# Kernel tuning notes

Measured on AMD Instinct MI355X. Metric: run time of the kernel, lower is better.

## Reference

```python
import jax, jax.numpy as jnp
import numpy as np
import math

N, MA, NFS, K, RC = 4, 256, 128, 8, 5.0
HID, OUT = 256, 32


def setup_inputs() -> dict:
    key = jax.random.key(0)
    ks = jax.random.split(key, 9)
    z = jax.random.randint(ks[0], (N, MA), 0, 10)
    r = jax.random.normal(ks[1], (N, MA, 3), dtype=jnp.float32) * 3.0
    h = jax.random.normal(ks[2], (N, MA, NFS), dtype=jnp.float32)
    Wa = jax.random.normal(ks[3], (2 * NFS, 1), dtype=jnp.float32) * 0.05
    ba = jnp.zeros((1,), dtype=jnp.float32)
    Wp1 = jax.random.normal(ks[4], (2 * NFS, HID), dtype=jnp.float32) * 0.05
    bp1 = jnp.zeros((HID,), dtype=jnp.float32)
    Wp2 = jax.random.normal(ks[5], (HID, OUT), dtype=jnp.float32) * 0.05
    bp2 = jnp.zeros((OUT,), dtype=jnp.float32)
    return {"z": z, "r": r, "h": h, "Wa": Wa, "ba": ba,
            "Wp1": Wp1, "bp1": bp1, "Wp2": Wp2, "bp2": bp2}


def reference(z, r, h, Wa, ba, Wp1, bp1, Wp2, bp2):
    n, ma = z.shape
    nfs = h.shape[2]
    # distance vectors dv[b,i,j] = r[b,j] - r[b,i]  -> [n, ma, ma, 3]
    dv = r[:, None, :, :] - r[:, :, None, :]
    d = jnp.linalg.norm(dv, axis=3)                       # [n, ma, ma]
    eye = jnp.eye(ma, dtype=jnp.float32)
    # cosine cutoff, zeroed on the diagonal
    cf = 0.5 * (jnp.cos(math.pi * jnp.minimum(d, RC) / RC) + 1.0)
    cf = (cf - eye[None])[..., None]                      # [n, ma, ma, 1]
    # pair validity mask (z > -1 marks real atoms), diagonal removed
    m = (z > -1).astype(jnp.float32)                      # [n, ma]
    mask = m[:, None, :] * m[:, :, None] - eye[None]
    mask = jnp.clip(mask, 0.0)[..., None]                 # [n, ma, ma, 1]
    cf = cf * mask
    # pairwise feature tensor u = [h_i, h_j * cf]         # [n, ma, ma, 2*nfs]
    u1 = jnp.broadcast_to(h[:, :, None, :], (n, ma, ma, nfs))
    u2 = h[:, None, :, :] * cf
    u = jnp.concatenate([u1, u2], axis=3)
    # exp attention, masked, normalized over neighbor axis (dim 2)
    g = (u @ Wa + ba) * mask                              # [n, ma, ma, 1]
    g = jnp.exp(g) - (1.0 - mask)
    attention = g / jnp.clip(g.sum(axis=2, keepdims=True), 1e-8)
    # top-k neighbors per query atom
    att, index = jax.lax.top_k(attention[..., 0], K)      # [n, ma, K]
    att = att[..., None]
    # gather neighbor features and distance vectors
    h2 = jnp.take_along_axis(h[:, None, :, :], index[..., None], axis=2)  # [n, ma, K, nfs]
    h1 = jnp.broadcast_to(h[:, :, None, :], (n, ma, K, nfs))
    uk = jnp.concatenate([h1, h2], axis=3) * att          # [n, ma, K, 2*nfs]
    dvk = jnp.take_along_axis(dv, index[..., None], axis=2)               # [n, ma, K, 3]
    dvk = dvk / jnp.clip(jnp.linalg.norm(dvk, axis=3, keepdims=True), 1e-4)
    dvk = dvk[:, :, :, None, :]                           # [n, ma, K, 1, 3]
    # pool MLP then cross with unit direction vectors
    c = jax.nn.silu(uk @ Wp1 + bp1) @ Wp2 + bp2           # [n, ma, K, OUT]
    c = c[..., None] * dvk                                # [n, ma, K, OUT, 3]
    return (z, r, c)
```

## Files before the change

kernel.cpp:

```cpp
#include <hip/hip_runtime.h>
#include <hip/hip_bf16.h>
#include <math.h>

#define NB 4
#define MA 256
#define NFS 128
#define KSEL 8
#define HID 256
#define NOUT 32
#define RCUT 5.0f
#define PI_F 3.14159265358979323846f

__global__ __launch_bounds__(256) void prep_kernel(
    const int* __restrict__ z, const float* __restrict__ r,
    const float* __restrict__ h, const float* __restrict__ Wa,
    const float* __restrict__ Wp1,
    float* __restrict__ out,
    float* __restrict__ a1, float* __restrict__ a2,
    float* __restrict__ P, float* __restrict__ Q) {
  const int b = blockIdx.x;
  const int half = b & 1;
  const int rg = b >> 1;
  const int r0 = 4 * rg;
  const int t = threadIdx.x;
  const int wave = t >> 6, lane = t & 63;
  const int c = t & 63, fq = t >> 6;

  __shared__ __align__(16) float hsh[4][NFS];
  __shared__ __align__(16) float psum[4][4][HID];

  ((float2*)hsh)[t] = ((const float2*)(h + (size_t)r0 * NFS))[t];
  __syncthreads();

  if (half == 0) {
    const float h0 = hsh[wave][lane], h1 = hsh[wave][lane + 64];
    float p1 = h0 * Wa[lane]       + h1 * Wa[lane + 64];
    float p2 = h0 * Wa[NFS + lane] + h1 * Wa[NFS + lane + 64];
#pragma unroll
    for (int off = 32; off > 0; off >>= 1) {
      p1 += __shfl_down(p1, off);
      p2 += __shfl_down(p2, off);
    }
    if (lane == 0) { a1[r0 + wave] = p1; a2[r0 + wave] = p2; }
    if (t < 4)  out[r0 + t] = (float)z[r0 + t];
    if (t < 12) out[NB * MA + r0 * 3 + t] = r[r0 * 3 + t];
  }

  const float* __restrict__ Wbase = Wp1 + (size_t)(half ? NFS : 0) * HID;
  float4 acc[4] = {make_float4(0,0,0,0), make_float4(0,0,0,0),
                   make_float4(0,0,0,0), make_float4(0,0,0,0)};
#pragma unroll 4
  for (int ff = 0; ff < 32; ++ff) {
    const int f = fq * 32 + ff;
    const float4 w = *(const float4*)&Wbase[(size_t)f * HID + 4 * c];
#pragma unroll
    for (int rr = 0; rr < 4; ++rr) {
      const float hv = hsh[rr][f];
      acc[rr].x = fmaf(hv, w.x, acc[rr].x);
      acc[rr].y = fmaf(hv, w.y, acc[rr].y);
      acc[rr].z = fmaf(hv, w.z, acc[rr].z);
      acc[rr].w = fmaf(hv, w.w, acc[rr].w);
    }
  }
#pragma unroll
  for (int rr = 0; rr < 4; ++rr) *(float4*)&psum[fq][rr][4 * c] = acc[rr];
  __syncthreads();

  {
    const int r2 = t >> 6, c2 = t & 63;
    float4 s = *(const float4*)&psum[0][r2][4 * c2];
#pragma unroll
    for (int q = 1; q < 4; ++q) {
      const float4 p = *(const float4*)&psum[q][r2][4 * c2];
      s.x += p.x; s.y += p.y; s.z += p.z; s.w += p.w;
    }
    float* dst = (half ? Q : P) + (size_t)(r0 + r2) * HID + 4 * c2;
    *(float4*)dst = s;
  }
}

__global__ __launch_bounds__(256) void main_kernel(
    const int* __restrict__ z, const float* __restrict__ r,
    const float* __restrict__ a1g, const float* __restrict__ a2g,
    const float* __restrict__ ba,
    const float* __restrict__ Pg, const float* __restrict__ Qg,
    const float* __restrict__ bp1,
    const float* __restrict__ Wp2g, const float* __restrict__ bp2,
    float* __restrict__ out) {
  const int row = blockIdx.x;
  const int n = row >> 8;
  const int i = row & 255;
  const int tid = threadIdx.x;
  const int lane = tid & 63;

  __shared__ float gsh[MA];
  __shared__ __align__(16) float hid_sh[KSEL][HID];
  __shared__ float psum2[8][KSEL][NOUT];

  const int l2o = tid & 31;
  const int l2c = tid >> 5;
  float wreg[32];
#pragma unroll
  for (int j = 0; j < 32; ++j) wreg[j] = Wp2g[(size_t)(32 * l2c + j) * NOUT + l2o];

  const float rix = r[row * 3 + 0], riy = r[row * 3 + 1], riz = r[row * 3 + 2];
  {
    const int jg = n * MA + tid;
    const float dx = r[jg * 3 + 0] - rix;
    const float dy = r[jg * 3 + 1] - riy;
    const float dz = r[jg * 3 + 2] - riz;
    const float d = sqrtf(dx * dx + dy * dy + dz * dz);
    const int mi = (z[row] > -1) ? 1 : 0;
    const int mj = (z[jg] > -1) ? 1 : 0;
    const int mask = max(mi * mj - ((tid == i) ? 1 : 0), 0);
    float g = 0.0f;
    if (mask) {
      const float cf = 0.5f * (__cosf(PI_F * fminf(d, RCUT) / RCUT) + 1.0f);
      g = __expf(a1g[row] + cf * a2g[jg] + ba[0]);
    }
    gsh[tid] = g;
  }
  __syncthreads();

  float att[KSEL];
  int   idx[KSEL];
  {
    float v0 = gsh[lane];
    float v1 = gsh[lane + 64];
    float v2 = gsh[lane + 128];
    float v3 = gsh[lane + 192];
    float s = (v0 + v1) + (v2 + v3);
#pragma unroll
    for (int off = 32; off > 0; off >>= 1) s += __shfl_xor(s, off);
    const float rden = 1.0f / fmaxf(s, 1e-8f);
#pragma unroll
    for (int k = 0; k < KSEL; k++) {
      float bv = v0; int bi = lane;
      if (v1 > bv) { bv = v1; bi = lane + 64; }
      if (v2 > bv) { bv = v2; bi = lane + 128; }
      if (v3 > bv) { bv = v3; bi = lane + 192; }
#pragma unroll
      for (int off = 32; off > 0; off >>= 1) {
        const float ov = __shfl_xor(bv, off);
        const int oi = __shfl_xor(bi, off);
        if (ov > bv || (ov == bv && oi < bi)) { bv = ov; bi = oi; }
      }
      att[k] = bv * rden;
      idx[k] = __builtin_amdgcn_readfirstlane(bi);
      const int slot = bi >> 6, who = bi & 63;
      if (lane == who) {
        if (slot == 0) v0 = -1.0f;
        else if (slot == 1) v1 = -1.0f;
        else if (slot == 2) v2 = -1.0f;
        else v3 = -1.0f;
      }
    }
  }

  {
    const float pi = Pg[(size_t)row * HID + tid];
    const float bb = bp1[tid];
#pragma unroll
    for (int k = 0; k < KSEL; k++) {
      const float q = Qg[(size_t)(n * MA + idx[k]) * HID + tid];
      const float x = att[k] * (pi + q) + bb;
      hid_sh[k][tid] = x / (1.0f + __expf(-x));
    }
  }
  __syncthreads();

  {
    float acc[KSEL];
#pragma unroll
    for (int k = 0; k < KSEL; ++k) acc[k] = 0.0f;
#pragma unroll
    for (int k = 0; k < KSEL; ++k) {
      const float4* __restrict__ hrow = (const float4*)&hid_sh[k][32 * l2c];
#pragma unroll
      for (int j4 = 0; j4 < 8; ++j4) {
        const float4 hv = hrow[j4];
        acc[k] = fmaf(hv.x, wreg[4 * j4 + 0],
                 fmaf(hv.y, wreg[4 * j4 + 1],
                 fmaf(hv.z, wreg[4 * j4 + 2],
                 fmaf(hv.w, wreg[4 * j4 + 3], acc[k]))));
      }
    }
#pragma unroll
    for (int k = 0; k < KSEL; ++k) psum2[l2c][k][l2o] = acc[k];
  }
  __syncthreads();

  {
    const int k2 = tid >> 5;
    const int o = tid & 31;
    float s = bp2[o];
#pragma unroll
    for (int cc = 0; cc < 8; ++cc) s += psum2[cc][k2][o];
    const int jg = n * MA + idx[k2];
    const float dx = r[jg * 3 + 0] - rix;
    const float dy = r[jg * 3 + 1] - riy;
    const float dz = r[jg * 3 + 2] - riz;
    const float nrm = fmaxf(sqrtf(dx * dx + dy * dy + dz * dz), 1e-4f);
    float* cb = out + NB * MA + NB * MA * 3 +
                ((size_t)row * KSEL + k2) * (NOUT * 3) + o * 3;
    cb[0] = s * (dx / nrm);
    cb[1] = s * (dy / nrm);
    cb[2] = s * (dz / nrm);
  }
}

extern "C" void kernel_launch(void* const* d_in, const int* in_sizes, int n_in,
                              void* d_out, int out_size, void* d_ws, size_t ws_size,
                              hipStream_t stream) {
  const int*   z   = (const int*)d_in[0];
  const float* r   = (const float*)d_in[1];
  const float* h   = (const float*)d_in[2];
  const float* Wa  = (const float*)d_in[3];
  const float* ba  = (const float*)d_in[4];
  const float* Wp1 = (const float*)d_in[5];
  const float* bp1 = (const float*)d_in[6];
  const float* Wp2 = (const float*)d_in[7];
  const float* bp2 = (const float*)d_in[8];
  float* out = (float*)d_out;

  float* a1 = (float*)d_ws;
  float* a2 = a1 + NB * MA;
  float* P  = a2 + NB * MA;
  float* Q  = P + (size_t)NB * MA * HID;

  prep_kernel<<<2 * NB * MA / 4, 256, 0, stream>>>(z, r, h, Wa, Wp1, out, a1, a2, P, Q);
  main_kernel<<<NB * MA, 256, 0, stream>>>(z, r, a1, a2, ba, P, Q, bp1, Wp2, bp2, out);
}
```

Baseline: 22.91 us.

## Double block counts in prep and main kernels by splitting columns and top-k halves

The prep kernel now splits each row group's output columns into two halves, giving four blocks per row group instead of two. The main kernel now launches two blocks per query row, and each block computes the MLP and output for four of the eight selected neighbors. The aim is more parallelism on a GPU with many CUs. In exchange, the attention scores, the softmax sum and the top-k selection are computed redundantly in both halves, and the second half still walks all eight selection rounds.

```diff
diff --git a/kernel.cpp b/kernel.cpp
--- a/kernel.cpp
+++ b/kernel.cpp
@@ -19,20 +19,21 @@
     float* __restrict__ a1, float* __restrict__ a2,
     float* __restrict__ P, float* __restrict__ Q) {
   const int b = blockIdx.x;
-  const int half = b & 1;
-  const int rg = b >> 1;
+  const int colhalf = b & 1;
+  const int pq = (b >> 1) & 1;
+  const int rg = b >> 2;
   const int r0 = 4 * rg;
   const int t = threadIdx.x;
   const int wave = t >> 6, lane = t & 63;
-  const int c = t & 63, fq = t >> 6;
+  const int c = t & 31, fq = t >> 5;
 
   __shared__ __align__(16) float hsh[4][NFS];
-  __shared__ __align__(16) float psum[4][4][HID];
+  __shared__ __align__(16) float psum[8][4][128];
 
   ((float2*)hsh)[t] = ((const float2*)(h + (size_t)r0 * NFS))[t];
   __syncthreads();
 
-  if (half == 0) {
+  if (pq == 0 && colhalf == 0) {
     const float h0 = hsh[wave][lane], h1 = hsh[wave][lane + 64];
     float p1 = h0 * Wa[lane]       + h1 * Wa[lane + 64];
     float p2 = h0 * Wa[NFS + lane] + h1 * Wa[NFS + lane + 64];
@@ -46,12 +47,12 @@
     if (t < 12) out[NB * MA + r0 * 3 + t] = r[r0 * 3 + t];
   }
 
-  const float* __restrict__ Wbase = Wp1 + (size_t)(half ? NFS : 0) * HID;
+  const float* __restrict__ Wbase = Wp1 + (size_t)(pq ? NFS : 0) * HID + colhalf * 128;
   float4 acc[4] = {make_float4(0,0,0,0), make_float4(0,0,0,0),
                    make_float4(0,0,0,0), make_float4(0,0,0,0)};
 #pragma unroll 4
-  for (int ff = 0; ff < 32; ++ff) {
-    const int f = fq * 32 + ff;
+  for (int ff = 0; ff < 16; ++ff) {
+    const int f = fq * 16 + ff;
     const float4 w = *(const float4*)&Wbase[(size_t)f * HID + 4 * c];
 #pragma unroll
     for (int rr = 0; rr < 4; ++rr) {
@@ -68,14 +69,14 @@
 
   {
     const int r2 = t >> 6, c2 = t & 63;
-    float4 s = *(const float4*)&psum[0][r2][4 * c2];
-#pragma unroll
-    for (int q = 1; q < 4; ++q) {
-      const float4 p = *(const float4*)&psum[q][r2][4 * c2];
-      s.x += p.x; s.y += p.y; s.z += p.z; s.w += p.w;
-    }
-    float* dst = (half ? Q : P) + (size_t)(r0 + r2) * HID + 4 * c2;
-    *(float4*)dst = s;
+    float2 s = *(const float2*)&psum[0][r2][2 * c2];
+#pragma unroll
+    for (int q = 1; q < 8; ++q) {
+      const float2 p = *(const float2*)&psum[q][r2][2 * c2];
+      s.x += p.x; s.y += p.y;
+    }
+    float* dst = (pq ? Q : P) + (size_t)(r0 + r2) * HID + colhalf * 128 + 2 * c2;
+    *(float2*)dst = s;
   }
 }
 
@@ -87,15 +88,17 @@
     const float* __restrict__ bp1,
     const float* __restrict__ Wp2g, const float* __restrict__ bp2,
     float* __restrict__ out) {
-  const int row = blockIdx.x;
+  const int row = blockIdx.x >> 1;
+  const int khalf = blockIdx.x & 1;
   const int n = row >> 8;
   const int i = row & 255;
   const int tid = threadIdx.x;
   const int lane = tid & 63;
 
   __shared__ float gsh[MA];
-  __shared__ __align__(16) float hid_sh[KSEL][HID];
-  __shared__ float psum2[8][KSEL][NOUT];
+  __shared__ __align__(16) float hid_sh[4][HID];
+  __shared__ float psum2[8][4][NOUT];
+  __shared__ int   idx_sh[4];
 
   const int l2o = tid & 31;
   const int l2c = tid >> 5;
@@ -122,8 +125,8 @@
   }
   __syncthreads();
 
-  float att[KSEL];
-  int   idx[KSEL];
+  float att4[4];
+  int   idx4[4];
   {
     float v0 = gsh[lane];
     float v1 = gsh[lane + 64];
@@ -135,46 +138,54 @@
     const float rden = 1.0f / fmaxf(s, 1e-8f);
 #pragma unroll
     for (int k = 0; k < KSEL; k++) {
-      float bv = v0; int bi = lane;
-      if (v1 > bv) { bv = v1; bi = lane + 64; }
-      if (v2 > bv) { bv = v2; bi = lane + 128; }
-      if (v3 > bv) { bv = v3; bi = lane + 192; }
-#pragma unroll
-      for (int off = 32; off > 0; off >>= 1) {
-        const float ov = __shfl_xor(bv, off);
-        const int oi = __shfl_xor(bi, off);
-        if (ov > bv || (ov == bv && oi < bi)) { bv = ov; bi = oi; }
+      if (k < 4 || khalf == 1) {
+        float bv = v0; int bi = lane;
+        if (v1 > bv) { bv = v1; bi = lane + 64; }
+        if (v2 > bv) { bv = v2; bi = lane + 128; }
+        if (v3 > bv) { bv = v3; bi = lane + 192; }
+#pragma unroll
+        for (int off = 32; off > 0; off >>= 1) {
+          const float ov = __shfl_xor(bv, off);
+          const int oi = __shfl_xor(bi, off);
+          if (ov > bv || (ov == bv && oi < bi)) { bv = ov; bi = oi; }
+        }
+        if ((k >> 2) == khalf) {
+          att4[k & 3] = bv * rden;
+          idx4[k & 3] = __builtin_amdgcn_readfirstlane(bi);
+        }
+        const int slot = bi >> 6, who = bi & 63;
+        if (lane == who) {
+          if (slot == 0) v0 = -1.0f;
+          else if (slot == 1) v1 = -1.0f;
+          else if (slot == 2) v2 = -1.0f;
+          else v3 = -1.0f;
+        }
       }
-      att[k] = bv * rden;
-      idx[k] = __builtin_amdgcn_readfirstlane(bi);
-      const int slot = bi >> 6, who = bi & 63;
-      if (lane == who) {
-        if (slot == 0) v0 = -1.0f;
-        else if (slot == 1) v1 = -1.0f;
-        else if (slot == 2) v2 = -1.0f;
-        else v3 = -1.0f;
-      }
-    }
+    }
+  }
+  if (lane == 0) {
+    idx_sh[0] = idx4[0]; idx_sh[1] = idx4[1];
+    idx_sh[2] = idx4[2]; idx_sh[3] = idx4[3];
   }
 
   {
     const float pi = Pg[(size_t)row * HID + tid];
     const float bb = bp1[tid];
 #pragma unroll
-    for (int k = 0; k < KSEL; k++) {
-      const float q = Qg[(size_t)(n * MA + idx[k]) * HID + tid];
-      const float x = att[k] * (pi + q) + bb;
+    for (int k = 0; k < 4; k++) {
+      const float q = Qg[(size_t)(n * MA + idx4[k]) * HID + tid];
+      const float x = att4[k] * (pi + q) + bb;
       hid_sh[k][tid] = x / (1.0f + __expf(-x));
     }
   }
   __syncthreads();
 
   {
-    float acc[KSEL];
-#pragma unroll
-    for (int k = 0; k < KSEL; ++k) acc[k] = 0.0f;
-#pragma unroll
-    for (int k = 0; k < KSEL; ++k) {
+    float acc[4];
+#pragma unroll
+    for (int k = 0; k < 4; ++k) acc[k] = 0.0f;
+#pragma unroll
+    for (int k = 0; k < 4; ++k) {
       const float4* __restrict__ hrow = (const float4*)&hid_sh[k][32 * l2c];
 #pragma unroll
       for (int j4 = 0; j4 < 8; ++j4) {
@@ -186,23 +197,23 @@
       }
     }
 #pragma unroll
-    for (int k = 0; k < KSEL; ++k) psum2[l2c][k][l2o] = acc[k];
-  }
-  __syncthreads();
-
-  {
+    for (int k = 0; k < 4; ++k) psum2[l2c][k][l2o] = acc[k];
+  }
+  __syncthreads();
+
+  if (tid < 128) {
     const int k2 = tid >> 5;
     const int o = tid & 31;
     float s = bp2[o];
 #pragma unroll
     for (int cc = 0; cc < 8; ++cc) s += psum2[cc][k2][o];
-    const int jg = n * MA + idx[k2];
+    const int jg = n * MA + idx_sh[k2];
     const float dx = r[jg * 3 + 0] - rix;
     const float dy = r[jg * 3 + 1] - riy;
     const float dz = r[jg * 3 + 2] - riz;
     const float nrm = fmaxf(sqrtf(dx * dx + dy * dy + dz * dz), 1e-4f);
     float* cb = out + NB * MA + NB * MA * 3 +
-                ((size_t)row * KSEL + k2) * (NOUT * 3) + o * 3;
+                ((size_t)row * KSEL + 4 * khalf + k2) * (NOUT * 3) + o * 3;
     cb[0] = s * (dx / nrm);
     cb[1] = s * (dy / nrm);
     cb[2] = s * (dz / nrm);
@@ -228,6 +239,6 @@
   float* P  = a2 + NB * MA;
   float* Q  = P + (size_t)NB * MA * HID;
 
-  prep_kernel<<<2 * NB * MA / 4, 256, 0, stream>>>(z, r, h, Wa, Wp1, out, a1, a2, P, Q);
-  main_kernel<<<NB * MA, 256, 0, stream>>>(z, r, a1, a2, ba, P, Q, bp1, Wp2, bp2, out);
+  prep_kernel<<<4 * (NB * MA / 4), 256, 0, stream>>>(z, r, h, Wa, Wp1, out, a1, a2, P, Q);
+  main_kernel<<<2 * NB * MA, 256, 0, stream>>>(z, r, a1, a2, ba, P, Q, bp1, Wp2, bp2, out);
 }
```

Result: slower. 26.98 us (+17.8%).

## Process two query rows per block in main kernel to amortize Wp2 loads

Applied to the files above, without the earlier changes.

Each block of main_kernel now handles two consecutive query atoms instead of one, halving the grid. The per-thread Wp2 register load, the r_j and mask loads, and the block launch overhead are shared across both rows, and the two top-k selections are interleaved to expose ILP in the shuffle reductions. Top-k indices are passed through shared memory for the final stage. The cost is more shared memory and registers per block and half as many blocks (512) to spread across the GPU's CUs.

```diff
diff --git a/kernel.cpp b/kernel.cpp
--- a/kernel.cpp
+++ b/kernel.cpp
@@ -87,15 +87,17 @@
     const float* __restrict__ bp1,
     const float* __restrict__ Wp2g, const float* __restrict__ bp2,
     float* __restrict__ out) {
-  const int row = blockIdx.x;
-  const int n = row >> 8;
-  const int i = row & 255;
+  const int rowA = blockIdx.x * 2;
+  const int rowB = rowA + 1;
+  const int n = rowA >> 8;
+  const int iA = rowA & 255, iB = rowB & 255;
   const int tid = threadIdx.x;
   const int lane = tid & 63;
 
-  __shared__ float gsh[MA];
-  __shared__ __align__(16) float hid_sh[KSEL][HID];
-  __shared__ float psum2[8][KSEL][NOUT];
+  __shared__ float gsh[2][MA];
+  __shared__ __align__(16) float hid_sh[2][KSEL][HID];
+  __shared__ float psum2[2][8][KSEL][NOUT];
+  __shared__ int   idx_sh[2][KSEL];
 
   const int l2o = tid & 31;
   const int l2c = tid >> 5;
@@ -103,109 +105,165 @@
 #pragma unroll
   for (int j = 0; j < 32; ++j) wreg[j] = Wp2g[(size_t)(32 * l2c + j) * NOUT + l2o];
 
-  const float rix = r[row * 3 + 0], riy = r[row * 3 + 1], riz = r[row * 3 + 2];
+  const float rAx = r[rowA * 3 + 0], rAy = r[rowA * 3 + 1], rAz = r[rowA * 3 + 2];
+  const float rBx = r[rowB * 3 + 0], rBy = r[rowB * 3 + 1], rBz = r[rowB * 3 + 2];
   {
     const int jg = n * MA + tid;
-    const float dx = r[jg * 3 + 0] - rix;
-    const float dy = r[jg * 3 + 1] - riy;
-    const float dz = r[jg * 3 + 2] - riz;
-    const float d = sqrtf(dx * dx + dy * dy + dz * dz);
-    const int mi = (z[row] > -1) ? 1 : 0;
+    const float rjx = r[jg * 3 + 0], rjy = r[jg * 3 + 1], rjz = r[jg * 3 + 2];
     const int mj = (z[jg] > -1) ? 1 : 0;
-    const int mask = max(mi * mj - ((tid == i) ? 1 : 0), 0);
-    float g = 0.0f;
-    if (mask) {
-      const float cf = 0.5f * (__cosf(PI_F * fminf(d, RCUT) / RCUT) + 1.0f);
-      g = __expf(a1g[row] + cf * a2g[jg] + ba[0]);
-    }
-    gsh[tid] = g;
-  }
-  __syncthreads();
-
-  float att[KSEL];
-  int   idx[KSEL];
-  {
-    float v0 = gsh[lane];
-    float v1 = gsh[lane + 64];
-    float v2 = gsh[lane + 128];
-    float v3 = gsh[lane + 192];
-    float s = (v0 + v1) + (v2 + v3);
-#pragma unroll
-    for (int off = 32; off > 0; off >>= 1) s += __shfl_xor(s, off);
-    const float rden = 1.0f / fmaxf(s, 1e-8f);
+    const int miA = (z[rowA] > -1) ? 1 : 0;
+    const int miB = (z[rowB] > -1) ? 1 : 0;
+    const float a2j = a2g[jg];
+    const float ba0 = ba[0];
+
+    const float dxA = rjx - rAx, dyA = rjy - rAy, dzA = rjz - rAz;
+    const float dA = sqrtf(dxA * dxA + dyA * dyA + dzA * dzA);
+    const int maskA = max(miA * mj - ((tid == iA) ? 1 : 0), 0);
+    float gA = 0.0f;
+    if (maskA) {
+      const float cf = 0.5f * (__cosf(PI_F * fminf(dA, RCUT) / RCUT) + 1.0f);
+      gA = __expf(a1g[rowA] + cf * a2j + ba0);
+    }
+    gsh[0][tid] = gA;
+
+    const float dxB = rjx - rBx, dyB = rjy - rBy, dzB = rjz - rBz;
+    const float dB = sqrtf(dxB * dxB + dyB * dyB + dzB * dzB);
+    const int maskB = max(miB * mj - ((tid == iB) ? 1 : 0), 0);
+    float gB = 0.0f;
+    if (maskB) {
+      const float cf = 0.5f * (__cosf(PI_F * fminf(dB, RCUT) / RCUT) + 1.0f);
+      gB = __expf(a1g[rowB] + cf * a2j + ba0);
+    }
+    gsh[1][tid] = gB;
+  }
+  __syncthreads();
+
+  float attA[KSEL], attB[KSEL];
+  int   idxA[KSEL], idxB[KSEL];
+  {
+    float v0A = gsh[0][lane],       v0B = gsh[1][lane];
+    float v1A = gsh[0][lane + 64],  v1B = gsh[1][lane + 64];
+    float v2A = gsh[0][lane + 128], v2B = gsh[1][lane + 128];
+    float v3A = gsh[0][lane + 192], v3B = gsh[1][lane + 192];
+    float sA = (v0A + v1A) + (v2A + v3A);
+    float sB = (v0B + v1B) + (v2B + v3B);
+#pragma unroll
+    for (int off = 32; off > 0; off >>= 1) {
+      sA += __shfl_xor(sA, off);
+      sB += __shfl_xor(sB, off);
+    }
+    const float rdenA = 1.0f / fmaxf(sA, 1e-8f);
+    const float rdenB = 1.0f / fmaxf(sB, 1e-8f);
 #pragma unroll
     for (int k = 0; k < KSEL; k++) {
-      float bv = v0; int bi = lane;
-      if (v1 > bv) { bv = v1; bi = lane + 64; }
-      if (v2 > bv) { bv = v2; bi = lane + 128; }
-      if (v3 > bv) { bv = v3; bi = lane + 192; }
+      float bvA = v0A; int biA = lane;
+      if (v1A > bvA) { bvA = v1A; biA = lane + 64; }
+      if (v2A > bvA) { bvA = v2A; biA = lane + 128; }
+      if (v3A > bvA) { bvA = v3A; biA = lane + 192; }
+      float bvB = v0B; int biB = lane;
+      if (v1B > bvB) { bvB = v1B; biB = lane + 64; }
+      if (v2B > bvB) { bvB = v2B; biB = lane + 128; }
+      if (v3B > bvB) { bvB = v3B; biB = lane + 192; }
 #pragma unroll
       for (int off = 32; off > 0; off >>= 1) {
-        const float ov = __shfl_xor(bv, off);
-        const int oi = __shfl_xor(bi, off);
-        if (ov > bv || (ov == bv && oi < bi)) { bv = ov; bi = oi; }
-      }
-      att[k] = bv * rden;
-      idx[k] = __builtin_amdgcn_readfirstlane(bi);
-      const int slot = bi >> 6, who = bi & 63;
-      if (lane == who) {
-        if (slot == 0) v0 = -1.0f;
-        else if (slot == 1) v1 = -1.0f;
-        else if (slot == 2) v2 = -1.0f;
-        else v3 = -1.0f;
-      }
-    }
-  }
-
-  {
-    const float pi = Pg[(size_t)row * HID + tid];
+        const float ovA = __shfl_xor(bvA, off);
+        const int   oiA = __shfl_xor(biA, off);
+        const float ovB = __shfl_xor(bvB, off);
+        const int   oiB = __shfl_xor(biB, off);
+        if (ovA > bvA || (ovA == bvA && oiA < biA)) { bvA = ovA; biA = oiA; }
+        if (ovB > bvB || (ovB == bvB && oiB < biB)) { bvB = ovB; biB = oiB; }
+      }
+      attA[k] = bvA * rdenA;
+      idxA[k] = __builtin_amdgcn_readfirstlane(biA);
+      attB[k] = bvB * rdenB;
+      idxB[k] = __builtin_amdgcn_readfirstlane(biB);
+      {
+        const int slot = biA >> 6, who = biA & 63;
+        if (lane == who) {
+          if (slot == 0) v0A = -1.0f;
+          else if (slot == 1) v1A = -1.0f;
+          else if (slot == 2) v2A = -1.0f;
+          else v3A = -1.0f;
+        }
+      }
+      {
+        const int slot = biB >> 6, who = biB & 63;
+        if (lane == who) {
+          if (slot == 0) v0B = -1.0f;
+          else if (slot == 1) v1B = -1.0f;
+          else if (slot == 2) v2B = -1.0f;
+          else v3B = -1.0f;
+        }
+      }
+    }
+  }
+  if (lane == 0) {
+#pragma unroll
+    for (int k = 0; k < KSEL; ++k) { idx_sh[0][k] = idxA[k]; idx_sh[1][k] = idxB[k]; }
+  }
+
+  {
+    const float pA = Pg[(size_t)rowA * HID + tid];
+    const float pB = Pg[(size_t)rowB * HID + tid];
     const float bb = bp1[tid];
 #pragma unroll
     for (int k = 0; k < KSEL; k++) {
-      const float q = Qg[(size_t)(n * MA + idx[k]) * HID + tid];
-      const float x = att[k] * (pi + q) + bb;
-      hid_sh[k][tid] = x / (1.0f + __expf(-x));
-    }
-  }
-  __syncthreads();
-
-  {
-    float acc[KSEL];
-#pragma unroll
-    for (int k = 0; k < KSEL; ++k) acc[k] = 0.0f;
-#pragma unroll
-    for (int k = 0; k < KSEL; ++k) {
-      const float4* __restrict__ hrow = (const float4*)&hid_sh[k][32 * l2c];
-#pragma unroll
-      for (int j4 = 0; j4 < 8; ++j4) {
-        const float4 hv = hrow[j4];
-        acc[k] = fmaf(hv.x, wreg[4 * j4 + 0],
-                 fmaf(hv.y, wreg[4 * j4 + 1],
-                 fmaf(hv.z, wreg[4 * j4 + 2],
-                 fmaf(hv.w, wreg[4 * j4 + 3], acc[k]))));
-      }
-    }
-#pragma unroll
-    for (int k = 0; k < KSEL; ++k) psum2[l2c][k][l2o] = acc[k];
+      const float qA = Qg[(size_t)(n * MA + idxA[k]) * HID + tid];
+      const float xA = attA[k] * (pA + qA) + bb;
+      hid_sh[0][k][tid] = xA / (1.0f + __expf(-xA));
+      const float qB = Qg[(size_t)(n * MA + idxB[k]) * HID + tid];
+      const float xB = attB[k] * (pB + qB) + bb;
+      hid_sh[1][k][tid] = xB / (1.0f + __expf(-xB));
+    }
+  }
+  __syncthreads();
+
+  {
+#pragma unroll
+    for (int rr = 0; rr < 2; ++rr) {
+      float acc[KSEL];
+#pragma unroll
+      for (int k = 0; k < KSEL; ++k) acc[k] = 0.0f;
+#pragma unroll
+      for (int k = 0; k < KSEL; ++k) {
+        const float4* __restrict__ hrow = (const float4*)&hid_sh[rr][k][32 * l2c];
+#pragma unroll
+        for (int j4 = 0; j4 < 8; ++j4) {
+          const float4 hv = hrow[j4];
+          acc[k] = fmaf(hv.x, wreg[4 * j4 + 0],
+                   fmaf(hv.y, wreg[4 * j4 + 1],
+                   fmaf(hv.z, wreg[4 * j4 + 2],
+                   fmaf(hv.w, wreg[4 * j4 + 3], acc[k]))));
+        }
+      }
+#pragma unroll
+      for (int k = 0; k < KSEL; ++k) psum2[rr][l2c][k][l2o] = acc[k];
+    }
   }
   __syncthreads();
 
   {
     const int k2 = tid >> 5;
     const int o = tid & 31;
-    float s = bp2[o];
-#pragma unroll
-    for (int cc = 0; cc < 8; ++cc) s += psum2[cc][k2][o];
-    const int jg = n * MA + idx[k2];
-    const float dx = r[jg * 3 + 0] - rix;
-    const float dy = r[jg * 3 + 1] - riy;
-    const float dz = r[jg * 3 + 2] - riz;
-    const float nrm = fmaxf(sqrtf(dx * dx + dy * dy + dz * dz), 1e-4f);
-    float* cb = out + NB * MA + NB * MA * 3 +
-                ((size_t)row * KSEL + k2) * (NOUT * 3) + o * 3;
-    cb[0] = s * (dx / nrm);
-    cb[1] = s * (dy / nrm);
-    cb[2] = s * (dz / nrm);
+#pragma unroll
+    for (int rr = 0; rr < 2; ++rr) {
+      float s = bp2[o];
+#pragma unroll
+      for (int cc = 0; cc < 8; ++cc) s += psum2[rr][cc][k2][o];
+      const int jg = n * MA + idx_sh[rr][k2];
+      const float rix = rr ? rBx : rAx;
+      const float riy = rr ? rBy : rAy;
+      const float riz = rr ? rBz : rAz;
+      const float dx = r[jg * 3 + 0] - rix;
+      const float dy = r[jg * 3 + 1] - riy;
+      const float dz = r[jg * 3 + 2] - riz;
+      const float nrm = fmaxf(sqrtf(dx * dx + dy * dy + dz * dz), 1e-4f);
+      float* cb = out + NB * MA + NB * MA * 3 +
+                  ((size_t)(rowA + rr) * KSEL + k2) * (NOUT * 3) + o * 3;
+      cb[0] = s * (dx / nrm);
+      cb[1] = s * (dy / nrm);
+      cb[2] = s * (dz / nrm);
+    }
   }
 }
 
@@ -229,5 +287,5 @@
   float* Q  = P + (size_t)NB * MA * HID;
 
   prep_kernel<<<2 * NB * MA / 4, 256, 0, stream>>>(z, r, h, Wa, Wp1, out, a1, a2, P, Q);
-  main_kernel<<<NB * MA, 256, 0, stream>>>(z, r, a1, a2, ba, P, Q, bp1, Wp2, bp2, out);
+  main_kernel<<<NB * MA / 2, 256, 0, stream>>>(z, r, a1, a2, ba, P, Q, bp1, Wp2, bp2, out);
 }
```

After: 26.73 us. 16.7% more time.

## Split main kernel into top-k kernel and half-K MLP kernel

Applied to the files above, without the earlier changes.

Splits the fused per-row kernel into a top-k kernel that writes attention weights and indices to workspace, and an MLP kernel launched with two blocks per row, each handling four of the eight neighbors. The aim is to stop three idle waves from holding the block during the single-wave top-k phase and to double the block count for the MLP stage. The cost is an extra kernel launch, a global round trip for the top-k results, and reloading Wp2 into registers in twice as many blocks.

```diff
diff --git a/kernel.cpp b/kernel.cpp
--- a/kernel.cpp
+++ b/kernel.cpp
@@ -79,29 +79,19 @@
   }
 }
 
-__global__ __launch_bounds__(256) void main_kernel(
+__global__ __launch_bounds__(256) void topk_kernel(
     const int* __restrict__ z, const float* __restrict__ r,
     const float* __restrict__ a1g, const float* __restrict__ a2g,
     const float* __restrict__ ba,
-    const float* __restrict__ Pg, const float* __restrict__ Qg,
-    const float* __restrict__ bp1,
-    const float* __restrict__ Wp2g, const float* __restrict__ bp2,
-    float* __restrict__ out) {
+    float* __restrict__ attw, int* __restrict__ idxw) {
   const int row = blockIdx.x;
   const int n = row >> 8;
   const int i = row & 255;
   const int tid = threadIdx.x;
   const int lane = tid & 63;
+  const int wave = tid >> 6;
 
   __shared__ float gsh[MA];
-  __shared__ __align__(16) float hid_sh[KSEL][HID];
-  __shared__ float psum2[8][KSEL][NOUT];
-
-  const int l2o = tid & 31;
-  const int l2c = tid >> 5;
-  float wreg[32];
-#pragma unroll
-  for (int j = 0; j < 32; ++j) wreg[j] = Wp2g[(size_t)(32 * l2c + j) * NOUT + l2o];
 
   const float rix = r[row * 3 + 0], riy = r[row * 3 + 1], riz = r[row * 3 + 2];
   {
@@ -121,6 +111,7 @@
     gsh[tid] = g;
   }
   __syncthreads();
+  if (wave != 0) return;
 
   float att[KSEL];
   int   idx[KSEL];
@@ -156,25 +147,61 @@
       }
     }
   }
+  if (lane == 0) {
+#pragma unroll
+    for (int k = 0; k < KSEL; ++k) {
+      attw[row * KSEL + k] = att[k];
+      idxw[row * KSEL + k] = idx[k];
+    }
+  }
+}
+
+__global__ __launch_bounds__(256) void mlp_kernel(
+    const float* __restrict__ r,
+    const float* __restrict__ Pg, const float* __restrict__ Qg,
+    const float* __restrict__ bp1,
+    const float* __restrict__ Wp2g, const float* __restrict__ bp2,
+    const float* __restrict__ attw, const int* __restrict__ idxw,
+    float* __restrict__ out) {
+  const int row = blockIdx.x >> 1;
+  const int khalf = blockIdx.x & 1;
+  const int n = row >> 8;
+  const int tid = threadIdx.x;
+
+  __shared__ __align__(16) float hid_sh[4][HID];
+  __shared__ float psum2[8][4][NOUT];
+
+  float att4[4]; int idx4[4];
+#pragma unroll
+  for (int k = 0; k < 4; ++k) {
+    att4[k] = attw[row * KSEL + 4 * khalf + k];
+    idx4[k] = idxw[row * KSEL + 4 * khalf + k];
+  }
+
+  const int l2o = tid & 31;
+  const int l2c = tid >> 5;
+  float wreg[32];
+#pragma unroll
+  for (int j = 0; j < 32; ++j) wreg[j] = Wp2g[(size_t)(32 * l2c + j) * NOUT + l2o];
 
   {
     const float pi = Pg[(size_t)row * HID + tid];
     const float bb = bp1[tid];
 #pragma unroll
-    for (int k = 0; k < KSEL; k++) {
-      const float q = Qg[(size_t)(n * MA + idx[k]) * HID + tid];
-      const float x = att[k] * (pi + q) + bb;
+    for (int k = 0; k < 4; k++) {
+      const float q = Qg[(size_t)(n * MA + idx4[k]) * HID + tid];
+      const float x = att4[k] * (pi + q) + bb;
       hid_sh[k][tid] = x / (1.0f + __expf(-x));
     }
   }
   __syncthreads();
 
   {
-    float acc[KSEL];
-#pragma unroll
-    for (int k = 0; k < KSEL; ++k) acc[k] = 0.0f;
-#pragma unroll
-    for (int k = 0; k < KSEL; ++k) {
+    float acc[4];
+#pragma unroll
+    for (int k = 0; k < 4; ++k) acc[k] = 0.0f;
+#pragma unroll
+    for (int k = 0; k < 4; ++k) {
       const float4* __restrict__ hrow = (const float4*)&hid_sh[k][32 * l2c];
 #pragma unroll
       for (int j4 = 0; j4 < 8; ++j4) {
@@ -186,23 +213,24 @@
       }
     }
 #pragma unroll
-    for (int k = 0; k < KSEL; ++k) psum2[l2c][k][l2o] = acc[k];
-  }
-  __syncthreads();
-
-  {
+    for (int k = 0; k < 4; ++k) psum2[l2c][k][l2o] = acc[k];
+  }
+  __syncthreads();
+
+  if (tid < 128) {
     const int k2 = tid >> 5;
     const int o = tid & 31;
     float s = bp2[o];
 #pragma unroll
     for (int cc = 0; cc < 8; ++cc) s += psum2[cc][k2][o];
-    const int jg = n * MA + idx[k2];
+    const float rix = r[row * 3 + 0], riy = r[row * 3 + 1], riz = r[row * 3 + 2];
+    const int jg = n * MA + idx4[k2];
     const float dx = r[jg * 3 + 0] - rix;
     const float dy = r[jg * 3 + 1] - riy;
     const float dz = r[jg * 3 + 2] - riz;
     const float nrm = fmaxf(sqrtf(dx * dx + dy * dy + dz * dz), 1e-4f);
     float* cb = out + NB * MA + NB * MA * 3 +
-                ((size_t)row * KSEL + k2) * (NOUT * 3) + o * 3;
+                ((size_t)row * KSEL + 4 * khalf + k2) * (NOUT * 3) + o * 3;
     cb[0] = s * (dx / nrm);
     cb[1] = s * (dy / nrm);
     cb[2] = s * (dz / nrm);
@@ -223,11 +251,14 @@
   const float* bp2 = (const float*)d_in[8];
   float* out = (float*)d_out;
 
-  float* a1 = (float*)d_ws;
-  float* a2 = a1 + NB * MA;
-  float* P  = a2 + NB * MA;
-  float* Q  = P + (size_t)NB * MA * HID;
+  float* a1   = (float*)d_ws;
+  float* a2   = a1 + NB * MA;
+  float* P    = a2 + NB * MA;
+  float* Q    = P + (size_t)NB * MA * HID;
+  float* attw = Q + (size_t)NB * MA * HID;
+  int*   idxw = (int*)(attw + NB * MA * KSEL);
 
   prep_kernel<<<2 * NB * MA / 4, 256, 0, stream>>>(z, r, h, Wa, Wp1, out, a1, a2, P, Q);
-  main_kernel<<<NB * MA, 256, 0, stream>>>(z, r, a1, a2, ba, P, Q, bp1, Wp2, bp2, out);
-}
+  topk_kernel<<<NB * MA, 256, 0, stream>>>(z, r, a1, a2, ba, attw, idxw);
+  mlp_kernel<<<2 * NB * MA, 256, 0, stream>>>(r, P, Q, bp1, Wp2, bp2, attw, idxw, out);
+}
```

Measured after the change: 23.74 us. 3.6% more time.
